# Kernel optimization log

Measured on AMD Instinct MI355X. Metric: run time of the kernel, lower is better.

The kernel has to match this reference:

```python
import jax, jax.numpy as jnp
import numpy as np

T, B, A, I, H, L = 256, 64, 512, 1024, 1024, 2
STDV = 1.0 / np.sqrt(H)

def _uniform(key, shape):
    return jax.random.uniform(key, shape, jnp.float32, -STDV, STDV)

def setup_inputs() -> dict:
    key = jax.random.key(0)
    ks = jax.random.split(key, 11)
    return {
        "attention": jax.random.normal(ks[0], (T, B, A), jnp.float32),
        "x": jax.random.normal(ks[1], (T, B, I), jnp.float32),
        "ping": jax.random.normal(ks[2], (B,), jnp.float32),  # unused by module
        "h0": jax.random.normal(ks[3], (L, B, H), jnp.float32),
        "c0": jax.random.normal(ks[4], (L, B, H), jnp.float32),
        "weight_ah": _uniform(ks[5], (L, A, 4 * H)),
        "weight_ih": _uniform(ks[6], (L, I, 4 * H)),  # input_size == hidden_size so layers stack
        "weight_hh": _uniform(ks[7], (L, H, 4 * H)),
        "bias_ah": _uniform(ks[8], (L, 4 * H)),
        "bias_ih": _uniform(ks[9], (L, 4 * H)),
        "bias_hh": _uniform(ks[10], (L, 4 * H)),
    }

def reference(attention, x, ping, h0, c0, weight_ah, weight_ih, weight_hh, bias_ah, bias_ih, bias_hh):
    # Faithful to SACILSTM.forward: only attention[0] is used (fixed across t),
    # ping is unused; per layer l, state is initialized from init_states[l].
    a0 = attention[0]  # [B, A]
    inputs = x  # [T, B, I]
    h_lasts, c_lasts = [], []
    for l in range(h0.shape[0]):
        w_hh = weight_hh[l]
        # Precompute the time-invariant + input-dependent part of the gates.
        const = a0 @ weight_ah[l] + bias_ah[l] + bias_ih[l] + bias_hh[l]  # [B, 4H]
        xg = jnp.einsum('tbi,ij->tbj', inputs, weight_ih[l]) + const  # [T, B, 4H]

        def step(carry, xg_t):
            h, c = carry
            gates = xg_t + h @ w_hh
            i_g, f_g, g_g, o_g = jnp.split(gates, 4, axis=-1)
            c = jax.nn.sigmoid(f_g) * c + jax.nn.sigmoid(i_g) * jnp.tanh(g_g)
            h = jax.nn.sigmoid(o_g) * jnp.tanh(c)
            return (h, c), h

        (h_T, c_T), hs = jax.lax.scan(step, (h0[l], c0[l]), xg)
        inputs = hs  # [T, B, H] feeds next layer
        h_lasts.append(h_T)
        c_lasts.append(c_T)
    # (self.h[:, -1], (self.h[-1], self.c[-1])) flattened
    return hs, jnp.stack(h_lasts), jnp.stack(c_lasts)
```

## Files before the change

### kernel.cpp

```cpp
#include <hip/hip_runtime.h>
#include <hip/hip_bf16.h>
#include <stdint.h>

#define TT 256
#define BB 64
#define AA 512
#define II 1024
#define HH 1024
#define LL 2
#define BH 65536
#define B4H 262144
#define OUT_HL 16777216
#define OUT_CL (16777216 + 131072)
#define NBLK 256

typedef __attribute__((ext_vector_type(8))) short bf16x8;
typedef __attribute__((ext_vector_type(4))) float f32x4;
typedef __attribute__((ext_vector_type(4))) unsigned int u32x4;
typedef __attribute__((ext_vector_type(2))) unsigned int u32x2;

__device__ __forceinline__ ushort f2bf(float v) {
    union { float f; uint32_t u; } x; x.f = v;
    uint32_t r = x.u + 0x7fff + ((x.u >> 16) & 1);
    return (ushort)(r >> 16);
}

__device__ __forceinline__ float sigf(float x) {
    return 1.f / (1.f + __expf(-x));
}


__global__ __launch_bounds__(256) void k_prep_wt(const float* __restrict__ wih,
                                                 const float* __restrict__ whh,
                                                 ushort* __restrict__ Wt) {
    __shared__ ushort tile[64][65];
    const int l = blockIdx.z;
    const int k0 = blockIdx.x * 64;
    const int col0 = blockIdx.y * 64;
    const int tid = threadIdx.x;
    const int cl = tid & 63, ks = tid >> 6;
    const float* src;
    int krow0;
    if (k0 < 1024) { src = wih + (size_t)l * 1024 * 4096; krow0 = k0; }
    else           { src = whh + (size_t)l * 1024 * 4096; krow0 = k0 - 1024; }
#pragma unroll
    for (int i = 0; i < 16; ++i) {
        int kl = ks + i * 4;
        tile[kl][cl] = f2bf(src[(size_t)(krow0 + kl) * 4096 + col0 + cl]);
    }
    __syncthreads();
    const int g0 = col0 >> 10, ub = col0 & 1023;
    ushort* dst = Wt + (size_t)l * 4096 * 2048;
    const int klane = tid & 63;
#pragma unroll
    for (int i = 0; i < 16; ++i) {
        int cl2 = (tid >> 6) + i * 4;
        int row = (ub + cl2) * 4 + g0;
        ushort* p = dst + (size_t)row * 2048 + k0 + klane;
        uint v = (uint)tile[klane][cl2];
        asm volatile("global_store_short %0, %1, off sc0 sc1"
                     :: "v"(p), "v"(v) : "memory");
    }
}

__global__ __launch_bounds__(256) void k_cast_x(const float* __restrict__ x,
                                                ushort* __restrict__ xbfF) {
    int i = blockIdx.x * 256 + threadIdx.x;
    int k8 = i & 127, b = (i >> 7) & 63, t = i >> 13;
    const float4* xs = (const float4*)(x + (((size_t)t * 64 + b) * 1024 + k8 * 8));
    float4 a = xs[0], c = xs[1];
    uint4 pk;
    pk.x = (uint)f2bf(a.x) | ((uint)f2bf(a.y) << 16);
    pk.y = (uint)f2bf(a.z) | ((uint)f2bf(a.w) << 16);
    pk.z = (uint)f2bf(c.x) | ((uint)f2bf(c.y) << 16);
    pk.w = (uint)f2bf(c.z) | ((uint)f2bf(c.w) << 16);
    size_t off = (size_t)t * 65536 + (size_t)(b >> 4) * 16384 +
                 (size_t)(k8 >> 2) * 512 + (size_t)(k8 & 3) * 128 + (size_t)(b & 15) * 8;
    *(uint4*)(xbfF + off) = pk;
}

__global__ __launch_bounds__(256) void k_const(const float* __restrict__ attn,
                                               const float* __restrict__ wah,
                                               const float* __restrict__ bah,
                                               const float* __restrict__ bih,
                                               const float* __restrict__ bhh,
                                               float* __restrict__ constg) {
    const int tid = threadIdx.x;
    const int col = blockIdx.x * 256 + tid;
    const int b0 = blockIdx.y * 8;
    const int l = blockIdx.z;
    const float* W = wah + (size_t)l * 512 * 4096;
    float acc[8] = {0.f, 0.f, 0.f, 0.f, 0.f, 0.f, 0.f, 0.f};
    for (int k = 0; k < 512; ++k) {
        float wv = W[(size_t)k * 4096 + col];
#pragma unroll
        for (int j = 0; j < 8; ++j) acc[j] += attn[(b0 + j) * 512 + k] * wv;
    }
    float bias = bah[l * 4096 + col] + bih[l * 4096 + col] + bhh[l * 4096 + col];
    float* cg = constg + (size_t)l * B4H;
#pragma unroll
    for (int j = 0; j < 8; ++j) cg[(size_t)(b0 + j) * 4096 + col] = acc[j] + bias;
}

__global__ __launch_bounds__(256) void k_init(const float* __restrict__ h0,
                                              ushort* __restrict__ hs0F,
                                              ushort* __restrict__ h1s0,
                                              unsigned* __restrict__ flags) {
    int i = blockIdx.x * 256 + threadIdx.x;
    if (i < 16384) {
        int k8 = i & 127, b = (i >> 7) & 63, l = i >> 13;
        const float* src = h0 + ((size_t)(l * 64 + b) * 1024 + k8 * 8);
        uint4 pk;
        pk.x = (uint)f2bf(src[0]) | ((uint)f2bf(src[1]) << 16);
        pk.y = (uint)f2bf(src[2]) | ((uint)f2bf(src[3]) << 16);
        pk.z = (uint)f2bf(src[4]) | ((uint)f2bf(src[5]) << 16);
        pk.w = (uint)f2bf(src[6]) | ((uint)f2bf(src[7]) << 16);
        size_t off = (size_t)(b >> 4) * 16384 + (size_t)(k8 >> 2) * 512 +
                     (size_t)(k8 & 3) * 128 + (size_t)(b & 15) * 8;
        *(uint4*)((l == 0 ? hs0F : h1s0) + off) = pk;
    }
    if (i < NBLK) flags[i] = 0u;
}

#define ISSUE(BUF, BASE)                                                       \
    do {                                                                       \
        _Pragma("unroll")                                                      \
        for (int _i = 0; _i < 8; ++_i)                                         \
            asm volatile("global_load_dwordx4 %0, %1, off"                     \
                         : "=v"(BUF[_i]) : "v"((BASE) + _i * 512));            \
    } while (0)

#define CHUNK(BUF, KTG0, N, A0, A1)                                            \
    do {                                                                       \
        asm volatile("s_waitcnt vmcnt(" #N ")" ::: "memory");                  \
        __builtin_amdgcn_sched_barrier(0x100);                                 \
        _Pragma("unroll")                                                      \
        for (int _i = 0; _i < 8; ++_i) {                                       \
            int _ktg = (KTG0) + _i;                                            \
            bf16x8 _b0 = *(const bf16x8*)(wlds + (size_t)_ktg * 1024 + lane * 8);       \
            bf16x8 _b1 = *(const bf16x8*)(wlds + (size_t)_ktg * 1024 + 512 + lane * 8); \
            A0 = __builtin_amdgcn_mfma_f32_16x16x32_bf16(BUF[_i], _b0, A0, 0, 0, 0);    \
            A1 = __builtin_amdgcn_mfma_f32_16x16x32_bf16(BUF[_i], _b1, A1, 0, 0, 0);    \
        }                                                                      \
    } while (0)

#define POLL128(FB, TGT)                                                       \
    do {                                                                       \
        const unsigned* _fp = (FB) + lane * 2;                                 \
        while (true) {                                                         \
            u32x2 _f;                                                          \
            asm volatile("global_load_dwordx2 %0, %1, off sc0 sc1\n\t"         \
                         "s_waitcnt vmcnt(0)"                                  \
                         : "=v"(_f) : "v"(_fp) : "memory");                    \
            if (__all(_f.x >= (TGT) && _f.y >= (TGT))) break;                  \
            __builtin_amdgcn_s_sleep(1);                                       \
        }                                                                      \
    } while (0)

__global__ __launch_bounds__(512, 2) void k_persist(
        const ushort* __restrict__ xbfF,
        ushort* __restrict__ hs0F,
        const ushort* __restrict__ h1s0,
        ushort* Wt,
        const float* __restrict__ constg,
        const float* __restrict__ c0,
        float* __restrict__ out,
        unsigned* __restrict__ flags) {
    __shared__ ushort wlds[65536];
    __shared__ float gt[2][4][2][16][18];

    const int tid = threadIdx.x;
    const int w = tid >> 6, lane = tid & 63;
    const int kh = w >> 2, m = w & 3;
    const int bid = blockIdx.x;
    const int layer = bid >> 7, ub = bid & 127;
    const int u0g = ub * 8;

    {
        bf16x8 vst[16];
#pragma unroll
        for (int i = 0; i < 16; ++i) {
            int c = i * 512 + tid;
            int lp = c & 63, nt = (c >> 6) & 1, ktg = c >> 7;
            int colp = u0g * 4 + nt * 16 + (lp & 15);
            int kk = ktg * 32 + (lp >> 4) * 8;
            const ushort* src = Wt + ((size_t)(layer * 4096 + colp)) * 2048 + kk;
            asm volatile("global_load_dwordx4 %0, %1, off sc0 sc1"
                         : "=v"(vst[i]) : "v"(src));
        }
        asm volatile("s_waitcnt vmcnt(0)" ::: "memory");
        __builtin_amdgcn_sched_barrier(0);
#pragma unroll
        for (int i = 0; i < 16; ++i) {
            int c = i * 512 + tid;
            *(bf16x8*)(wlds + (size_t)c * 8) = vst[i];
        }
    }

    const int b_e = (w << 3) | (lane >> 3);
    const int u_off = lane & 7;
    const int u_e = u0g + u_off;
    float cg[4];
#pragma unroll
    for (int g = 0; g < 4; ++g)
        cg[g] = constg[(size_t)layer * B4H + (size_t)b_e * 4096 + g * 1024 + u_e];
    float creg = c0[layer * BH + b_e * 1024 + u_e];
    const int mb = b_e >> 4, blb = b_e & 15, ntb = u_off >> 2, cpb = (u_off & 3) * 4;
    const size_t hoffL = (size_t)mb * 16384 + (size_t)(ub >> 2) * 512 +
                         (size_t)(ub & 3) * 128 + (size_t)blb * 8;

    const size_t fro = (size_t)m * 16384 + (size_t)lane * 8;

    __syncthreads();

    const int sBeg = layer ? 1 : 0;
    const int sEnd = layer ? TT : (TT - 1);
    for (int s = sBeg; s <= sEnd; ++s) {
        const int t1 = s - 1;
        bf16x8 bufA[8], bufB[8], bufC[8], bufD[8];
        f32x4 aE0 = {0.f,0.f,0.f,0.f}, aO0 = {0.f,0.f,0.f,0.f};
        f32x4 aE1 = {0.f,0.f,0.f,0.f}, aO1 = {0.f,0.f,0.f,0.f};

        if (layer == 0) {
            {
                const ushort* ax = xbfF + (size_t)s * 65536 + fro + kh * 8192;
                ISSUE(bufA, ax);
                ISSUE(bufB, ax + 4096);
                CHUNK(bufA, kh * 16,     8, aE0, aE1);
                CHUNK(bufB, kh * 16 + 8, 0, aO0, aO1);
            }
            if (s >= 1 && w == 0) POLL128(flags, (unsigned)s);
            __syncthreads();
            {
                const ushort* ah = hs0F + (size_t)s * 65536 + fro + kh * 8192;
                ISSUE(bufA, ah);
                ISSUE(bufB, ah + 4096);
                CHUNK(bufA, 32 + kh * 16,     8, aE0, aE1);
                CHUNK(bufB, 32 + kh * 16 + 8, 0, aO0, aO1);
            }
        } else {
            if (w == 0) POLL128(flags, (unsigned)s);
            if (w == 4 && s >= 2) POLL128(flags + 128, (unsigned)s);
            __syncthreads();
            {
                const ushort* a = (kh == 0)
                    ? hs0F + (size_t)s * 65536 + fro
                    : (t1 == 0 ? h1s0 + fro
                               : (const ushort*)Wt + (size_t)(t1 - 1) * 65536 + fro);
                ISSUE(bufA, a);
                ISSUE(bufB, a + 4096);
                ISSUE(bufC, a + 8192);
                ISSUE(bufD, a + 12288);
                CHUNK(bufA, kh * 32,      24, aE0, aE1);
                CHUNK(bufB, kh * 32 + 8,  16, aO0, aO1);
                CHUNK(bufC, kh * 32 + 16,  8, aE0, aE1);
                CHUNK(bufD, kh * 32 + 24,  0, aO0, aO1);
            }
        }

        {
            const int cc = lane & 15, r0 = (lane >> 4) * 4;
#pragma unroll
            for (int r = 0; r < 4; ++r) {
                gt[kh][m][0][r0 + r][cc] = aE0[r] + aO0[r];
                gt[kh][m][1][r0 + r][cc] = aE1[r] + aO1[r];
            }
        }
        __syncthreads();

        float g4[4];
#pragma unroll
        for (int g = 0; g < 4; ++g)
            g4[g] = gt[0][mb][ntb][blb][cpb + g] + gt[1][mb][ntb][blb][cpb + g] + cg[g];
        float si = sigf(g4[0]), sf = sigf(g4[1]), so = sigf(g4[3]);
        float cn = sf * creg + si * (2.f * sigf(2.f * g4[2]) - 1.f);
        float hv = so * (2.f * sigf(2.f * cn) - 1.f);
        creg = cn;
        uint hb = (uint)f2bf(hv);
        uint p0 = __shfl(hb, (lane & 56) + 0), p1 = __shfl(hb, (lane & 56) + 1);
        uint p2 = __shfl(hb, (lane & 56) + 2), p3 = __shfl(hb, (lane & 56) + 3);
        uint p4 = __shfl(hb, (lane & 56) + 4), p5 = __shfl(hb, (lane & 56) + 5);
        uint p6 = __shfl(hb, (lane & 56) + 6), p7 = __shfl(hb, (lane & 56) + 7);
        u32x4 hp;
        hp.x = (p0 & 0xffffu) | (p1 << 16);
        hp.y = (p2 & 0xffffu) | (p3 << 16);
        hp.z = (p4 & 0xffffu) | (p5 << 16);
        hp.w = (p6 & 0xffffu) | (p7 << 16);
        ushort* hdst = (layer ? Wt + (size_t)t1 * 65536
                              : hs0F + (size_t)(s + 1) * 65536) + hoffL;
        if (u_off == 0)
            asm volatile("global_store_dwordx4 %0, %1, off sc0 sc1"
                         :: "v"(hdst), "v"(hp) : "memory");

        asm volatile("s_waitcnt vmcnt(0)" ::: "memory");
        __syncthreads();
        if (tid == 0) {
            unsigned tgt = (unsigned)(s + 1);
            unsigned* fp = flags + layer * 128 + ub;
            asm volatile("global_store_dword %0, %1, off sc0 sc1"
                         :: "v"(fp), "v"(tgt) : "memory");
        }

        if (layer == 1) {
            float o0 = __shfl(hv, (lane & 56) + 0), o1 = __shfl(hv, (lane & 56) + 1);
            float o2 = __shfl(hv, (lane & 56) + 2), o3 = __shfl(hv, (lane & 56) + 3);
            float o4 = __shfl(hv, (lane & 56) + 4), o5 = __shfl(hv, (lane & 56) + 5);
            float o6 = __shfl(hv, (lane & 56) + 6), o7 = __shfl(hv, (lane & 56) + 7);
            if (u_off == 0) {
                float* op = out + (size_t)t1 * 65536 + (size_t)b_e * 1024 + u0g;
                float4 v0 = {o0, o1, o2, o3}, v1 = {o4, o5, o6, o7};
                *(float4*)op = v0;
                *(float4*)(op + 4) = v1;
            }
            if (t1 == TT - 1) {
                out[OUT_HL + BH + b_e * 1024 + u_e] = hv;
                out[OUT_CL + BH + b_e * 1024 + u_e] = cn;
            }
        } else if (s == TT - 1) {
            out[OUT_HL + b_e * 1024 + u_e] = hv;
            out[OUT_CL + b_e * 1024 + u_e] = cn;
        }
    }
}

extern "C" void kernel_launch(void* const* d_in, const int* in_sizes, int n_in,
                              void* d_out, int out_size, void* d_ws, size_t ws_size,
                              hipStream_t stream) {
    const float* attn = (const float*)d_in[0];
    const float* x    = (const float*)d_in[1];
    const float* h0   = (const float*)d_in[3];
    const float* c0   = (const float*)d_in[4];
    const float* wah  = (const float*)d_in[5];
    const float* wih  = (const float*)d_in[6];
    const float* whh  = (const float*)d_in[7];
    const float* bah  = (const float*)d_in[8];
    const float* bih  = (const float*)d_in[9];
    const float* bhh  = (const float*)d_in[10];
    float* out = (float*)d_out;

    char* ws = (char*)d_ws;
    ushort*   Wt     = (ushort*)(ws);
    ushort*   xbfF   = (ushort*)(ws + 33554432);
    ushort*   hs0F   = (ushort*)(ws + 67108864);
    ushort*   h1s0   = (ushort*)(ws + 100794368);
    float*    constg = (float*)(ws + 100925440);
    unsigned* flags  = (unsigned*)(ws + 103022592);

    hipLaunchKernelGGL(k_prep_wt, dim3(32, 64, 2), dim3(256), 0, stream, wih, whh, Wt);
    hipLaunchKernelGGL(k_cast_x, dim3(8192), dim3(256), 0, stream, x, xbfF);
    hipLaunchKernelGGL(k_const, dim3(16, 8, 2), dim3(256), 0, stream, attn, wah, bah, bih, bhh, constg);
    hipLaunchKernelGGL(k_init, dim3(64), dim3(256), 0, stream, h0, hs0F, h1s0, flags);

    void* args[] = { (void*)&xbfF, (void*)&hs0F, (void*)&h1s0, (void*)&Wt,
                     (void*)&constg, (void*)&c0, (void*)&out, (void*)&flags };
    hipLaunchCooperativeKernel((void*)k_persist, dim3(NBLK), dim3(512), args, 0, stream);
}
```

Baseline: 1.681 ms.

## Split persistent LSTM into four roles, decoupling input-projection blocks from recurrent blocks

The persistent kernel now gives 256 blocks four roles: input-projection producers for each layer (x@Wih and h0@Wih) that write fp32 gate partials into ring buffers, and recurrent blocks that only compute h@Whh and the cell update. Weights are loaded into shared memory once at kernel start. The ring buffers reuse the Wt workspace region, and new flag arrays handle ring-slot backpressure and a startup barrier so blocks only overwrite Wt after every block has loaded its weights. The intent is to take the input GEMM off the serial recurrent critical path so each recurrent step does half the K-work. The cost is more flag polling, extra global traffic for the fp32 partials, and fragile ordering around the aliased workspace.

Measured after the change: 2.199 ms. 1.31x slower.

```diff
diff --git a/kernel.cpp b/kernel.cpp
--- a/kernel.cpp
+++ b/kernel.cpp
@@ -3,31 +3,24 @@
 #include <stdint.h>
 
 #define TT 256
-#define BB 64
-#define AA 512
-#define II 1024
-#define HH 1024
-#define LL 2
 #define BH 65536
 #define B4H 262144
 #define OUT_HL 16777216
 #define OUT_CL (16777216 + 131072)
 #define NBLK 256
+#define SLAB 65536
+#define XGSZ 262144
 
 typedef __attribute__((ext_vector_type(8))) short bf16x8;
 typedef __attribute__((ext_vector_type(4))) float f32x4;
 typedef __attribute__((ext_vector_type(4))) unsigned int u32x4;
-typedef __attribute__((ext_vector_type(2))) unsigned int u32x2;
 
 __device__ __forceinline__ ushort f2bf(float v) {
     union { float f; uint32_t u; } x; x.f = v;
     uint32_t r = x.u + 0x7fff + ((x.u >> 16) & 1);
     return (ushort)(r >> 16);
 }
-
-__device__ __forceinline__ float sigf(float x) {
-    return 1.f / (1.f + __expf(-x));
-}
+__device__ __forceinline__ float sigf(float x) { return 1.f / (1.f + __expf(-x)); }
 
 
 __global__ __launch_bounds__(256) void k_prep_wt(const float* __restrict__ wih,
@@ -74,7 +67,7 @@
     pk.y = (uint)f2bf(a.z) | ((uint)f2bf(a.w) << 16);
     pk.z = (uint)f2bf(c.x) | ((uint)f2bf(c.y) << 16);
     pk.w = (uint)f2bf(c.z) | ((uint)f2bf(c.w) << 16);
-    size_t off = (size_t)t * 65536 + (size_t)(b >> 4) * 16384 +
+    size_t off = (size_t)t * SLAB + (size_t)(b >> 4) * 16384 +
                  (size_t)(k8 >> 2) * 512 + (size_t)(k8 & 3) * 128 + (size_t)(b & 15) * 8;
     *(uint4*)(xbfF + off) = pk;
 }
@@ -119,72 +112,98 @@
                      (size_t)(k8 & 3) * 128 + (size_t)(b & 15) * 8;
         *(uint4*)((l == 0 ? hs0F : h1s0) + off) = pk;
     }
-    if (i < NBLK) flags[i] = 0u;
-}
-
-#define ISSUE(BUF, BASE)                                                       \
-    do {                                                                       \
-        _Pragma("unroll")                                                      \
+    if (i < 512) flags[i] = 0u;
+}
+
+#define ISSUE8(BUF, BASE)                                                      \
+    do { _Pragma("unroll")                                                     \
         for (int _i = 0; _i < 8; ++_i)                                         \
             asm volatile("global_load_dwordx4 %0, %1, off"                     \
-                         : "=v"(BUF[_i]) : "v"((BASE) + _i * 512));            \
-    } while (0)
-
-#define CHUNK(BUF, KTG0, N, A0, A1)                                            \
+                         : "=v"(BUF[_i]) : "v"((BASE) + _i * 512)); } while (0)
+#define ISSUE8_SC(BUF, BASE)                                                   \
+    do { _Pragma("unroll")                                                     \
+        for (int _i = 0; _i < 8; ++_i)                                         \
+            asm volatile("global_load_dwordx4 %0, %1, off sc0 sc1"             \
+                         : "=v"(BUF[_i]) : "v"((BASE) + _i * 512)); } while (0)
+
+#define MFMA(A, B, C) __builtin_amdgcn_mfma_f32_16x16x32_bf16(A, B, C, 0, 0, 0)
+
+#define CHUNK8(BUF, KTG0, N)                                                   \
     do {                                                                       \
         asm volatile("s_waitcnt vmcnt(" #N ")" ::: "memory");                  \
         __builtin_amdgcn_sched_barrier(0x100);                                 \
         _Pragma("unroll")                                                      \
         for (int _i = 0; _i < 8; ++_i) {                                       \
-            int _ktg = (KTG0) + _i;                                            \
-            bf16x8 _b0 = *(const bf16x8*)(wlds + (size_t)_ktg * 1024 + lane * 8);       \
-            bf16x8 _b1 = *(const bf16x8*)(wlds + (size_t)_ktg * 1024 + 512 + lane * 8); \
-            A0 = __builtin_amdgcn_mfma_f32_16x16x32_bf16(BUF[_i], _b0, A0, 0, 0, 0);    \
-            A1 = __builtin_amdgcn_mfma_f32_16x16x32_bf16(BUF[_i], _b1, A1, 0, 0, 0);    \
+            const ushort* _wb = wlds + ((size_t)((KTG0) + _i) * 256 + lane) * 8; \
+            bf16x8 _b0 = *(const bf16x8*)(_wb);                                \
+            bf16x8 _b1 = *(const bf16x8*)(_wb + 512);                          \
+            bf16x8 _b2 = *(const bf16x8*)(_wb + 1024);                         \
+            bf16x8 _b3 = *(const bf16x8*)(_wb + 1536);                         \
+            acc0 = MFMA(BUF[_i], _b0, acc0);                                   \
+            acc1 = MFMA(BUF[_i], _b1, acc1);                                   \
+            acc2 = MFMA(BUF[_i], _b2, acc2);                                   \
+            acc3 = MFMA(BUF[_i], _b3, acc3);                                   \
         }                                                                      \
     } while (0)
 
-#define POLL128(FB, TGT)                                                       \
-    do {                                                                       \
-        const unsigned* _fp = (FB) + lane * 2;                                 \
-        while (true) {                                                         \
-            u32x2 _f;                                                          \
-            asm volatile("global_load_dwordx2 %0, %1, off sc0 sc1\n\t"         \
-                         "s_waitcnt vmcnt(0)"                                  \
-                         : "=v"(_f) : "v"(_fp) : "memory");                    \
-            if (__all(_f.x >= (TGT) && _f.y >= (TGT))) break;                  \
-            __builtin_amdgcn_s_sleep(1);                                       \
-        }                                                                      \
-    } while (0)
+#define POLLALL64(FB, TGT)                                                     \
+    do { const unsigned* _fp = (FB) + lane;                                    \
+        while (true) { unsigned _f;                                            \
+            asm volatile("global_load_dword %0, %1, off sc0 sc1\n\t"           \
+                         "s_waitcnt vmcnt(0)" : "=v"(_f) : "v"(_fp) : "memory"); \
+            if (__all(_f >= (unsigned)(TGT))) break;                           \
+            __builtin_amdgcn_s_sleep(1); } } while (0)
+
+#define POLLONE(FP, TGT)                                                       \
+    do { while (true) { unsigned _f;                                           \
+            asm volatile("global_load_dword %0, %1, off sc0 sc1\n\t"           \
+                         "s_waitcnt vmcnt(0)" : "=v"(_f) : "v"(FP) : "memory"); \
+            if (_f >= (unsigned)(TGT)) break;                                  \
+            __builtin_amdgcn_s_sleep(1); } } while (0)
+
+#define POLLS256(FB)                                                           \
+    do { const unsigned* _fp = (FB) + lane * 4;                                \
+        while (true) { u32x4 _f;                                               \
+            asm volatile("global_load_dwordx4 %0, %1, off sc0 sc1\n\t"         \
+                         "s_waitcnt vmcnt(0)" : "=v"(_f) : "v"(_fp) : "memory"); \
+            if (__all(_f.x && _f.y && _f.z && _f.w)) break;                    \
+            __builtin_amdgcn_s_sleep(1); } } while (0)
 
 __global__ __launch_bounds__(512, 2) void k_persist(
-        const ushort* __restrict__ xbfF,
-        ushort* __restrict__ hs0F,
+        ushort* xbfF,
+        ushort* hs0F,
         const ushort* __restrict__ h1s0,
-        ushort* Wt,
+        const ushort* __restrict__ Wt,
         const float* __restrict__ constg,
         const float* __restrict__ c0,
         float* __restrict__ out,
-        unsigned* __restrict__ flags) {
+        unsigned* flags,
+        float* xg0, float* xg1) {
     __shared__ ushort wlds[65536];
-    __shared__ float gt[2][4][2][16][18];
+    __shared__ float gt[4][16][68];
 
     const int tid = threadIdx.x;
     const int w = tid >> 6, lane = tid & 63;
     const int kh = w >> 2, m = w & 3;
     const int bid = blockIdx.x;
-    const int layer = bid >> 7, ub = bid & 127;
-    const int u0g = ub * 8;
+    const int role = bid >> 6, j = bid & 63;
+    const int lsel = role >> 1;
+    const int hbase = (role & 1) * 1024;
+    unsigned* fS  = flags;
+    unsigned* fAp = flags + 256;
+    unsigned* fA  = flags + 320;
+    unsigned* fB  = flags + 384;
+    unsigned* fC  = flags + 448;
 
     {
         bf16x8 vst[16];
 #pragma unroll
         for (int i = 0; i < 16; ++i) {
             int c = i * 512 + tid;
-            int lp = c & 63, nt = (c >> 6) & 1, ktg = c >> 7;
-            int colp = u0g * 4 + nt * 16 + (lp & 15);
-            int kk = ktg * 32 + (lp >> 4) * 8;
-            const ushort* src = Wt + ((size_t)(layer * 4096 + colp)) * 2048 + kk;
+            int ktg = c >> 8, nt = (c >> 6) & 3, lp = c & 63;
+            int colp = 64 * j + nt * 16 + (lp & 15);
+            int kk = hbase + ktg * 32 + (lp >> 4) * 8;
+            const ushort* src = Wt + ((size_t)(lsel * 4096 + colp)) * 2048 + kk;
             asm volatile("global_load_dwordx4 %0, %1, off sc0 sc1"
                          : "=v"(vst[i]) : "v"(src));
         }
@@ -196,129 +215,174 @@
             *(bf16x8*)(wlds + (size_t)c * 8) = vst[i];
         }
     }
-
-    const int b_e = (w << 3) | (lane >> 3);
-    const int u_off = lane & 7;
-    const int u_e = u0g + u_off;
-    float cg[4];
-#pragma unroll
-    for (int g = 0; g < 4; ++g)
-        cg[g] = constg[(size_t)layer * B4H + (size_t)b_e * 4096 + g * 1024 + u_e];
-    float creg = c0[layer * BH + b_e * 1024 + u_e];
-    const int mb = b_e >> 4, blb = b_e & 15, ntb = u_off >> 2, cpb = (u_off & 3) * 4;
-    const size_t hoffL = (size_t)mb * 16384 + (size_t)(ub >> 2) * 512 +
-                         (size_t)(ub & 3) * 128 + (size_t)blb * 8;
-
-    const size_t fro = (size_t)m * 16384 + (size_t)lane * 8;
-
     __syncthreads();
-
-    const int sBeg = layer ? 1 : 0;
-    const int sEnd = layer ? TT : (TT - 1);
-    for (int s = sBeg; s <= sEnd; ++s) {
-        const int t1 = s - 1;
-        bf16x8 bufA[8], bufB[8], bufC[8], bufD[8];
-        f32x4 aE0 = {0.f,0.f,0.f,0.f}, aO0 = {0.f,0.f,0.f,0.f};
-        f32x4 aE1 = {0.f,0.f,0.f,0.f}, aO1 = {0.f,0.f,0.f,0.f};
-
-        if (layer == 0) {
-            {
-                const ushort* ax = xbfF + (size_t)s * 65536 + fro + kh * 8192;
-                ISSUE(bufA, ax);
-                ISSUE(bufB, ax + 4096);
-                CHUNK(bufA, kh * 16,     8, aE0, aE1);
-                CHUNK(bufB, kh * 16 + 8, 0, aO0, aO1);
-            }
-            if (s >= 1 && w == 0) POLL128(flags, (unsigned)s);
-            __syncthreads();
-            {
-                const ushort* ah = hs0F + (size_t)s * 65536 + fro + kh * 8192;
-                ISSUE(bufA, ah);
-                ISSUE(bufB, ah + 4096);
-                CHUNK(bufA, 32 + kh * 16,     8, aE0, aE1);
-                CHUNK(bufB, 32 + kh * 16 + 8, 0, aO0, aO1);
+    if (tid == 0) {
+        unsigned one = 1u; unsigned* fp = fS + bid;
+        asm volatile("global_store_dword %0, %1, off sc0 sc1"
+                     :: "v"(fp), "v"(one) : "memory");
+    }
+
+    const int cc = lane & 15, r0 = (lane >> 4) * 4;
+    f32x4 cst0 = {0,0,0,0}, cst1 = {0,0,0,0}, cst2 = {0,0,0,0}, cst3 = {0,0,0,0};
+    if (role == 0 || role == 2) {
+#pragma unroll
+        for (int nt = 0; nt < 4; ++nt) {
+            int colp = nt * 16 + cc;
+            size_t base = (size_t)lsel * B4H + (size_t)(cc & 3) * 1024 + 16 * j + (colp >> 2);
+            f32x4 v;
+#pragma unroll
+            for (int r = 0; r < 4; ++r)
+                v[r] = constg[base + (size_t)(m * 16 + r0 + r) * 4096];
+            if (nt == 0) cst0 = v; else if (nt == 1) cst1 = v;
+            else if (nt == 2) cst2 = v; else cst3 = v;
+        }
+    }
+    const int b_e = tid >> 3, p_e = tid & 7, up = p_e * 2;
+    const int ug0 = 16 * j + up;
+    float cregA = 0.f, cregB = 0.f;
+    size_t hoffT = 0;
+    if (role == 1 || role == 3) {
+        cregA = c0[lsel * BH + b_e * 1024 + ug0];
+        cregB = c0[lsel * BH + b_e * 1024 + ug0 + 1];
+        hoffT = (size_t)(b_e >> 4) * 16384 + (size_t)(ug0 >> 5) * 512 +
+                (size_t)((ug0 >> 3) & 3) * 128 + (size_t)(b_e & 15) * 8 + (ug0 & 7);
+    }
+    const size_t fro = (size_t)m * 16384 + (size_t)(kh * 16) * 512 + (size_t)lane * 8;
+    __syncthreads();
+
+    for (int t = 0; t < TT; ++t) {
+        f32x4 acc0 = {0,0,0,0}, acc1 = {0,0,0,0}, acc2 = {0,0,0,0}, acc3 = {0,0,0,0};
+        bf16x8 bufA[8], bufB[8];
+        float xgv[8];
+
+        if (role == 1) {
+            if (w == 0) POLLALL64(fA, t);
+            if (w == 1) POLLONE(fAp + j, t + 1);
+            __syncthreads();
+        } else if (role == 2) {
+            if (w == 0) POLLALL64(fA, t + 1);
+            if (w == 1 && t >= 7) POLLONE(fC + j, t - 6);
+            __syncthreads();
+        } else if (role == 3) {
+            if (w == 0) POLLALL64(fC, t);
+            if (w == 1) POLLONE(fB + j, t + 1);
+            __syncthreads();
+        }
+
+        if (role == 1 || role == 3) {
+            const float* xg = (role == 1) ? xg0 + (size_t)(t & 15) * XGSZ
+                                          : xg1 + (size_t)(t & 7) * XGSZ;
+#pragma unroll
+            for (int e = 0; e < 2; ++e)
+#pragma unroll
+                for (int g = 0; g < 4; ++g) {
+                    const float* p = xg + (size_t)((64 * j + (up + e) * 4 + g)) * 64 + b_e;
+                    asm volatile("global_load_dword %0, %1, off sc0 sc1"
+                                 : "=v"(xgv[e * 4 + g]) : "v"(p));
+                }
+        }
+
+        {
+            const ushort* slab;
+            if (role == 0)      slab = xbfF + (size_t)t * SLAB;
+            else if (role == 1) slab = hs0F + (size_t)t * SLAB;
+            else if (role == 2) slab = hs0F + (size_t)(t + 1) * SLAB;
+            else                slab = (t == 0) ? h1s0 : xbfF + (size_t)(t - 1) * SLAB;
+            const ushort* base = slab + fro;
+            if (role == 0) { ISSUE8_SC(bufA, base); ISSUE8_SC(bufB, base + 4096); }
+            else           { ISSUE8(bufA, base);    ISSUE8(bufB, base + 4096); }
+            CHUNK8(bufA, kh * 16, 8);
+            CHUNK8(bufB, kh * 16 + 8, 0);
+        }
+
+        if (kh == 1) {
+#pragma unroll
+            for (int r = 0; r < 4; ++r) {
+                gt[m][r0 + r][0 * 16 + cc] = acc0[r];
+                gt[m][r0 + r][1 * 16 + cc] = acc1[r];
+                gt[m][r0 + r][2 * 16 + cc] = acc2[r];
+                gt[m][r0 + r][3 * 16 + cc] = acc3[r];
+            }
+        }
+        if (role == 0) {
+            if (w == 0 && t == 0) POLLS256(fS);
+            if (w == 0 && t >= 15) POLLONE(fA + j, t - 14);
+        }
+        __syncthreads();
+
+        if (role == 0 || role == 2) {
+            if (kh == 0) {
+                float* dst = (role == 0 ? xg0 + (size_t)(t & 15) * XGSZ
+                                        : xg1 + (size_t)(t & 7) * XGSZ);
+#pragma unroll
+                for (int nt = 0; nt < 4; ++nt) {
+                    f32x4 a = (nt == 0) ? acc0 : (nt == 1) ? acc1 : (nt == 2) ? acc2 : acc3;
+                    f32x4 cs = (nt == 0) ? cst0 : (nt == 1) ? cst1 : (nt == 2) ? cst2 : cst3;
+                    f32x4 v;
+#pragma unroll
+                    for (int r = 0; r < 4; ++r)
+                        v[r] = a[r] + gt[m][r0 + r][nt * 16 + cc] + cs[r];
+                    float* ap = dst + (size_t)(64 * j + nt * 16 + cc) * 64 + m * 16 + r0;
+                    asm volatile("global_store_dwordx4 %0, %1, off sc0 sc1"
+                                 :: "v"(ap), "v"(v) : "memory");
+                }
+            }
+            asm volatile("s_waitcnt vmcnt(0)" ::: "memory");
+            __syncthreads();
+            if (tid == 0) {
+                unsigned tgt = (unsigned)(t + 1);
+                unsigned* fp = (role == 0 ? fAp : fB) + j;
+                asm volatile("global_store_dword %0, %1, off sc0 sc1"
+                             :: "v"(fp), "v"(tgt) : "memory");
             }
         } else {
-            if (w == 0) POLL128(flags, (unsigned)s);
-            if (w == 4 && s >= 2) POLL128(flags + 128, (unsigned)s);
-            __syncthreads();
-            {
-                const ushort* a = (kh == 0)
-                    ? hs0F + (size_t)s * 65536 + fro
-                    : (t1 == 0 ? h1s0 + fro
-                               : (const ushort*)Wt + (size_t)(t1 - 1) * 65536 + fro);
-                ISSUE(bufA, a);
-                ISSUE(bufB, a + 4096);
-                ISSUE(bufC, a + 8192);
-                ISSUE(bufD, a + 12288);
-                CHUNK(bufA, kh * 32,      24, aE0, aE1);
-                CHUNK(bufB, kh * 32 + 8,  16, aO0, aO1);
-                CHUNK(bufC, kh * 32 + 16,  8, aE0, aE1);
-                CHUNK(bufD, kh * 32 + 24,  0, aO0, aO1);
-            }
-        }
-
-        {
-            const int cc = lane & 15, r0 = (lane >> 4) * 4;
-#pragma unroll
-            for (int r = 0; r < 4; ++r) {
-                gt[kh][m][0][r0 + r][cc] = aE0[r] + aO0[r];
-                gt[kh][m][1][r0 + r][cc] = aE1[r] + aO1[r];
-            }
-        }
-        __syncthreads();
-
-        float g4[4];
-#pragma unroll
-        for (int g = 0; g < 4; ++g)
-            g4[g] = gt[0][mb][ntb][blb][cpb + g] + gt[1][mb][ntb][blb][cpb + g] + cg[g];
-        float si = sigf(g4[0]), sf = sigf(g4[1]), so = sigf(g4[3]);
-        float cn = sf * creg + si * (2.f * sigf(2.f * g4[2]) - 1.f);
-        float hv = so * (2.f * sigf(2.f * cn) - 1.f);
-        creg = cn;
-        uint hb = (uint)f2bf(hv);
-        uint p0 = __shfl(hb, (lane & 56) + 0), p1 = __shfl(hb, (lane & 56) + 1);
-        uint p2 = __shfl(hb, (lane & 56) + 2), p3 = __shfl(hb, (lane & 56) + 3);
-        uint p4 = __shfl(hb, (lane & 56) + 4), p5 = __shfl(hb, (lane & 56) + 5);
-        uint p6 = __shfl(hb, (lane & 56) + 6), p7 = __shfl(hb, (lane & 56) + 7);
-        u32x4 hp;
-        hp.x = (p0 & 0xffffu) | (p1 << 16);
-        hp.y = (p2 & 0xffffu) | (p3 << 16);
-        hp.z = (p4 & 0xffffu) | (p5 << 16);
-        hp.w = (p6 & 0xffffu) | (p7 << 16);
-        ushort* hdst = (layer ? Wt + (size_t)t1 * 65536
-                              : hs0F + (size_t)(s + 1) * 65536) + hoffL;
-        if (u_off == 0)
-            asm volatile("global_store_dwordx4 %0, %1, off sc0 sc1"
-                         :: "v"(hdst), "v"(hp) : "memory");
-
-        asm volatile("s_waitcnt vmcnt(0)" ::: "memory");
-        __syncthreads();
-        if (tid == 0) {
-            unsigned tgt = (unsigned)(s + 1);
-            unsigned* fp = flags + layer * 128 + ub;
+            if (kh == 0) {
+#pragma unroll
+                for (int r = 0; r < 4; ++r) {
+                    gt[m][r0 + r][0 * 16 + cc] += acc0[r];
+                    gt[m][r0 + r][1 * 16 + cc] += acc1[r];
+                    gt[m][r0 + r][2 * 16 + cc] += acc2[r];
+                    gt[m][r0 + r][3 * 16 + cc] += acc3[r];
+                }
+            }
+            __syncthreads();
+            f32x4 va = *(const f32x4*)&gt[b_e >> 4][b_e & 15][up * 4];
+            f32x4 vb = *(const f32x4*)&gt[b_e >> 4][b_e & 15][up * 4 + 4];
+            float giA = va[0] + xgv[0], gfA = va[1] + xgv[1];
+            float ggA = va[2] + xgv[2], goA = va[3] + xgv[3];
+            float giB = vb[0] + xgv[4], gfB = vb[1] + xgv[5];
+            float ggB = vb[2] + xgv[6], goB = vb[3] + xgv[7];
+            float cnA = sigf(gfA) * cregA + sigf(giA) * (2.f * sigf(2.f * ggA) - 1.f);
+            float hvA = sigf(goA) * (2.f * sigf(2.f * cnA) - 1.f);
+            float cnB = sigf(gfB) * cregB + sigf(giB) * (2.f * sigf(2.f * ggB) - 1.f);
+            float hvB = sigf(goB) * (2.f * sigf(2.f * cnB) - 1.f);
+            cregA = cnA; cregB = cnB;
+            uint hb = (uint)f2bf(hvA) | ((uint)f2bf(hvB) << 16);
+            ushort* hdst = (role == 1 ? hs0F + (size_t)(t + 1) * SLAB
+                                      : xbfF + (size_t)t * SLAB) + hoffT;
             asm volatile("global_store_dword %0, %1, off sc0 sc1"
-                         :: "v"(fp), "v"(tgt) : "memory");
-        }
-
-        if (layer == 1) {
-            float o0 = __shfl(hv, (lane & 56) + 0), o1 = __shfl(hv, (lane & 56) + 1);
-            float o2 = __shfl(hv, (lane & 56) + 2), o3 = __shfl(hv, (lane & 56) + 3);
-            float o4 = __shfl(hv, (lane & 56) + 4), o5 = __shfl(hv, (lane & 56) + 5);
-            float o6 = __shfl(hv, (lane & 56) + 6), o7 = __shfl(hv, (lane & 56) + 7);
-            if (u_off == 0) {
-                float* op = out + (size_t)t1 * 65536 + (size_t)b_e * 1024 + u0g;
-                float4 v0 = {o0, o1, o2, o3}, v1 = {o4, o5, o6, o7};
-                *(float4*)op = v0;
-                *(float4*)(op + 4) = v1;
-            }
-            if (t1 == TT - 1) {
-                out[OUT_HL + BH + b_e * 1024 + u_e] = hv;
-                out[OUT_CL + BH + b_e * 1024 + u_e] = cn;
-            }
-        } else if (s == TT - 1) {
-            out[OUT_HL + b_e * 1024 + u_e] = hv;
-            out[OUT_CL + b_e * 1024 + u_e] = cn;
+                         :: "v"(hdst), "v"(hb) : "memory");
+            asm volatile("s_waitcnt vmcnt(0)" ::: "memory");
+            __syncthreads();
+            if (tid == 0) {
+                unsigned tgt = (unsigned)(t + 1);
+                unsigned* fp = (role == 1 ? fA : fC) + j;
+                asm volatile("global_store_dword %0, %1, off sc0 sc1"
+                             :: "v"(fp), "v"(tgt) : "memory");
+            }
+            if (role == 3) {
+                float2 ov; ov.x = hvA; ov.y = hvB;
+                *(float2*)(out + (size_t)t * BH + (size_t)b_e * 1024 + ug0) = ov;
+                if (t == TT - 1) {
+                    int idx = b_e * 1024 + ug0;
+                    out[OUT_HL + BH + idx] = hvA; out[OUT_HL + BH + idx + 1] = hvB;
+                    out[OUT_CL + BH + idx] = cnA; out[OUT_CL + BH + idx + 1] = cnB;
+                }
+            } else if (t == TT - 1) {
+                int idx = b_e * 1024 + ug0;
+                out[OUT_HL + idx] = hvA; out[OUT_HL + idx + 1] = hvB;
+                out[OUT_CL + idx] = cnA; out[OUT_CL + idx + 1] = cnB;
+            }
         }
     }
 }
@@ -340,6 +404,8 @@
 
     char* ws = (char*)d_ws;
     ushort*   Wt     = (ushort*)(ws);
+    float*    xg0    = (float*)(ws);
+    float*    xg1    = (float*)(ws + 16777216);
     ushort*   xbfF   = (ushort*)(ws + 33554432);
     ushort*   hs0F   = (ushort*)(ws + 67108864);
     ushort*   h1s0   = (ushort*)(ws + 100794368);
@@ -352,6 +418,7 @@
     hipLaunchKernelGGL(k_init, dim3(64), dim3(256), 0, stream, h0, hs0F, h1s0, flags);
 
     void* args[] = { (void*)&xbfF, (void*)&hs0F, (void*)&h1s0, (void*)&Wt,
-                     (void*)&constg, (void*)&c0, (void*)&out, (void*)&flags };
+                     (void*)&constg, (void*)&c0, (void*)&out, (void*)&flags,
+                     (void*)&xg0, (void*)&xg1 };
     hipLaunchCooperativeKernel((void*)k_persist, dim3(NBLK), dim3(512), args, 0, stream);
 }
```

## Split LSTM recurrence per layer and prefetch next-step operands across barriers

Applied to the files above, without the earlier changes.

The persistent recurrent kernel is split into separate loops for layer 0 and layer 1. Each loop issues the loads for the next step's operands early: the next x slab in layer 0, and the freshly published layer-0 h in layer 1. This lets those loads overlap with the current step's MFMA work and flag polling, and the k-split is reorganized so each half reads input and recurrent operands in separate register buffers. It adds register pressure from four live buffer sets. The layer-1 waits are also restructured, with two separate polls per step, which could change synchronization latency.

After: 2.064 ms. +22.8%, slower.

```diff
diff --git a/kernel.cpp b/kernel.cpp
--- a/kernel.cpp
+++ b/kernel.cpp
@@ -3,16 +3,12 @@
 #include <stdint.h>
 
 #define TT 256
-#define BB 64
-#define AA 512
-#define II 1024
-#define HH 1024
-#define LL 2
 #define BH 65536
 #define B4H 262144
 #define OUT_HL 16777216
 #define OUT_CL (16777216 + 131072)
 #define NBLK 256
+#define SLAB 65536
 
 typedef __attribute__((ext_vector_type(8))) short bf16x8;
 typedef __attribute__((ext_vector_type(4))) float f32x4;
@@ -24,10 +20,7 @@
     uint32_t r = x.u + 0x7fff + ((x.u >> 16) & 1);
     return (ushort)(r >> 16);
 }
-
-__device__ __forceinline__ float sigf(float x) {
-    return 1.f / (1.f + __expf(-x));
-}
+__device__ __forceinline__ float sigf(float x) { return 1.f / (1.f + __expf(-x)); }
 
 
 __global__ __launch_bounds__(256) void k_prep_wt(const float* __restrict__ wih,
@@ -74,7 +67,7 @@
     pk.y = (uint)f2bf(a.z) | ((uint)f2bf(a.w) << 16);
     pk.z = (uint)f2bf(c.x) | ((uint)f2bf(c.y) << 16);
     pk.w = (uint)f2bf(c.z) | ((uint)f2bf(c.w) << 16);
-    size_t off = (size_t)t * 65536 + (size_t)(b >> 4) * 16384 +
+    size_t off = (size_t)t * SLAB + (size_t)(b >> 4) * 16384 +
                  (size_t)(k8 >> 2) * 512 + (size_t)(k8 & 3) * 128 + (size_t)(b & 15) * 8;
     *(uint4*)(xbfF + off) = pk;
 }
@@ -123,12 +116,10 @@
 }
 
 #define ISSUE(BUF, BASE)                                                       \
-    do {                                                                       \
-        _Pragma("unroll")                                                      \
+    do { _Pragma("unroll")                                                     \
         for (int _i = 0; _i < 8; ++_i)                                         \
             asm volatile("global_load_dwordx4 %0, %1, off"                     \
-                         : "=v"(BUF[_i]) : "v"((BASE) + _i * 512));            \
-    } while (0)
+                         : "=v"(BUF[_i]) : "v"((BASE) + _i * 512)); } while (0)
 
 #define CHUNK(BUF, KTG0, N, A0, A1)                                            \
     do {                                                                       \
@@ -209,116 +200,160 @@
     const size_t hoffL = (size_t)mb * 16384 + (size_t)(ub >> 2) * 512 +
                          (size_t)(ub & 3) * 128 + (size_t)blb * 8;
 
-    const size_t fro = (size_t)m * 16384 + (size_t)lane * 8;
+    const size_t fro = (size_t)m * 16384 + (size_t)(kh * 16) * 512 + (size_t)lane * 8;
+    unsigned* f0 = flags;
+    unsigned* f1 = flags + 128;
 
     __syncthreads();
 
-    const int sBeg = layer ? 1 : 0;
-    const int sEnd = layer ? TT : (TT - 1);
-    for (int s = sBeg; s <= sEnd; ++s) {
-        const int t1 = s - 1;
-        bf16x8 bufA[8], bufB[8], bufC[8], bufD[8];
-        f32x4 aE0 = {0.f,0.f,0.f,0.f}, aO0 = {0.f,0.f,0.f,0.f};
-        f32x4 aE1 = {0.f,0.f,0.f,0.f}, aO1 = {0.f,0.f,0.f,0.f};
-
-        if (layer == 0) {
+    bf16x8 bufXa[8], bufXb[8];
+    bf16x8 bufHa[8], bufHb[8];
+
+    if (layer == 0) {
+        { const ushort* ax = xbfF + fro; ISSUE(bufXa, ax); ISSUE(bufXb, ax + 4096); }
+        { const ushort* ah = hs0F + fro; ISSUE(bufHa, ah); ISSUE(bufHb, ah + 4096); }
+        for (int s = 0; s < TT; ++s) {
+            f32x4 aE0 = {0,0,0,0}, aO0 = {0,0,0,0};
+            f32x4 aE1 = {0,0,0,0}, aO1 = {0,0,0,0};
+            CHUNK(bufXa, kh * 16,     16, aE0, aE1);
+            CHUNK(bufXb, kh * 16 + 8, 16, aO0, aO1);
+            { const ushort* ax = xbfF + (size_t)((s + 1) & 255) * SLAB + fro;
+              ISSUE(bufXa, ax); ISSUE(bufXb, ax + 4096); }
+            CHUNK(bufHa, 32 + kh * 16,     24, aE0, aE1);
+            CHUNK(bufHb, 32 + kh * 16 + 8, 16, aO0, aO1);
             {
-                const ushort* ax = xbfF + (size_t)s * 65536 + fro + kh * 8192;
-                ISSUE(bufA, ax);
-                ISSUE(bufB, ax + 4096);
-                CHUNK(bufA, kh * 16,     8, aE0, aE1);
-                CHUNK(bufB, kh * 16 + 8, 0, aO0, aO1);
-            }
-            if (s >= 1 && w == 0) POLL128(flags, (unsigned)s);
+                const int cc = lane & 15, r0 = (lane >> 4) * 4;
+#pragma unroll
+                for (int r = 0; r < 4; ++r) {
+                    gt[kh][m][0][r0 + r][cc] = aE0[r] + aO0[r];
+                    gt[kh][m][1][r0 + r][cc] = aE1[r] + aO1[r];
+                }
+            }
             __syncthreads();
+            float g4[4];
+#pragma unroll
+            for (int g = 0; g < 4; ++g)
+                g4[g] = gt[0][mb][ntb][blb][cpb + g] + gt[1][mb][ntb][blb][cpb + g] + cg[g];
+            float si = sigf(g4[0]), sf = sigf(g4[1]), so = sigf(g4[3]);
+            float cn = sf * creg + si * (2.f * sigf(2.f * g4[2]) - 1.f);
+            float hv = so * (2.f * sigf(2.f * cn) - 1.f);
+            creg = cn;
+            uint hb = (uint)f2bf(hv);
+            uint p0 = __shfl(hb, (lane & 56) + 0), p1 = __shfl(hb, (lane & 56) + 1);
+            uint p2 = __shfl(hb, (lane & 56) + 2), p3 = __shfl(hb, (lane & 56) + 3);
+            uint p4 = __shfl(hb, (lane & 56) + 4), p5 = __shfl(hb, (lane & 56) + 5);
+            uint p6 = __shfl(hb, (lane & 56) + 6), p7 = __shfl(hb, (lane & 56) + 7);
+            u32x4 hp;
+            hp.x = (p0 & 0xffffu) | (p1 << 16);
+            hp.y = (p2 & 0xffffu) | (p3 << 16);
+            hp.z = (p4 & 0xffffu) | (p5 << 16);
+            hp.w = (p6 & 0xffffu) | (p7 << 16);
+            ushort* hdst = hs0F + (size_t)(s + 1) * SLAB + hoffL;
+            if (u_off == 0)
+                asm volatile("global_store_dwordx4 %0, %1, off sc0 sc1"
+                             :: "v"(hdst), "v"(hp) : "memory");
+            asm volatile("s_waitcnt vmcnt(0)" ::: "memory");
+            __syncthreads();
+            if (tid == 0) {
+                unsigned tgt = (unsigned)(s + 1);
+                unsigned* fp = f0 + ub;
+                asm volatile("global_store_dword %0, %1, off sc0 sc1"
+                             :: "v"(fp), "v"(tgt) : "memory");
+            }
+            if (s == TT - 1) {
+                int idx = b_e * 1024 + u_e;
+                out[OUT_HL + idx] = hv;
+                out[OUT_CL + idx] = cn;
+            }
+            if (s < TT - 1) {
+                if (w == 0) POLL128(f0, (unsigned)(s + 1));
+                __syncthreads();
+                const ushort* ah = hs0F + (size_t)(s + 1) * SLAB + fro;
+                ISSUE(bufHa, ah); ISSUE(bufHb, ah + 4096);
+            }
+        }
+    } else {
+        if (w == 0) POLL128(f0, 1u);
+        __syncthreads();
+        { const ushort* ah = hs0F + (size_t)1 * SLAB + fro;
+          ISSUE(bufHa, ah); ISSUE(bufHb, ah + 4096); }
+        for (int s = 1; s <= TT; ++s) {
+            const int t1 = s - 1;
+            f32x4 aE0 = {0,0,0,0}, aO0 = {0,0,0,0};
+            f32x4 aE1 = {0,0,0,0}, aO1 = {0,0,0,0};
+            if (s >= 2) {
+                if (w == 0) POLL128(f1, (unsigned)s);
+                __syncthreads();
+            }
+            { const ushort* ar = (t1 == 0 ? h1s0
+                                 : (const ushort*)Wt + (size_t)(t1 - 1) * SLAB) + fro;
+              ISSUE(bufXa, ar); ISSUE(bufXb, ar + 4096); }
+            CHUNK(bufHa, kh * 16,          24, aE0, aE1);
+            CHUNK(bufHb, kh * 16 + 8,      16, aO0, aO1);
+            CHUNK(bufXa, 32 + kh * 16,      8, aE0, aE1);
+            CHUNK(bufXb, 32 + kh * 16 + 8,  0, aO0, aO1);
             {
-                const ushort* ah = hs0F + (size_t)s * 65536 + fro + kh * 8192;
-                ISSUE(bufA, ah);
-                ISSUE(bufB, ah + 4096);
-                CHUNK(bufA, 32 + kh * 16,     8, aE0, aE1);
-                CHUNK(bufB, 32 + kh * 16 + 8, 0, aO0, aO1);
-            }
-        } else {
-            if (w == 0) POLL128(flags, (unsigned)s);
-            if (w == 4 && s >= 2) POLL128(flags + 128, (unsigned)s);
+                const int cc = lane & 15, r0 = (lane >> 4) * 4;
+#pragma unroll
+                for (int r = 0; r < 4; ++r) {
+                    gt[kh][m][0][r0 + r][cc] = aE0[r] + aO0[r];
+                    gt[kh][m][1][r0 + r][cc] = aE1[r] + aO1[r];
+                }
+            }
             __syncthreads();
+            float g4[4];
+#pragma unroll
+            for (int g = 0; g < 4; ++g)
+                g4[g] = gt[0][mb][ntb][blb][cpb + g] + gt[1][mb][ntb][blb][cpb + g] + cg[g];
+            float si = sigf(g4[0]), sf = sigf(g4[1]), so = sigf(g4[3]);
+            float cn = sf * creg + si * (2.f * sigf(2.f * g4[2]) - 1.f);
+            float hv = so * (2.f * sigf(2.f * cn) - 1.f);
+            creg = cn;
+            uint hb = (uint)f2bf(hv);
+            uint p0 = __shfl(hb, (lane & 56) + 0), p1 = __shfl(hb, (lane & 56) + 1);
+            uint p2 = __shfl(hb, (lane & 56) + 2), p3 = __shfl(hb, (lane & 56) + 3);
+            uint p4 = __shfl(hb, (lane & 56) + 4), p5 = __shfl(hb, (lane & 56) + 5);
+            uint p6 = __shfl(hb, (lane & 56) + 6), p7 = __shfl(hb, (lane & 56) + 7);
+            u32x4 hp;
+            hp.x = (p0 & 0xffffu) | (p1 << 16);
+            hp.y = (p2 & 0xffffu) | (p3 << 16);
+            hp.z = (p4 & 0xffffu) | (p5 << 16);
+            hp.w = (p6 & 0xffffu) | (p7 << 16);
+            ushort* hdst = Wt + (size_t)t1 * SLAB + hoffL;
+            if (u_off == 0)
+                asm volatile("global_store_dwordx4 %0, %1, off sc0 sc1"
+                             :: "v"(hdst), "v"(hp) : "memory");
+            asm volatile("s_waitcnt vmcnt(0)" ::: "memory");
+            __syncthreads();
+            if (tid == 0) {
+                unsigned tgt = (unsigned)(s + 1);
+                unsigned* fp = f1 + ub;
+                asm volatile("global_store_dword %0, %1, off sc0 sc1"
+                             :: "v"(fp), "v"(tgt) : "memory");
+            }
             {
-                const ushort* a = (kh == 0)
-                    ? hs0F + (size_t)s * 65536 + fro
-                    : (t1 == 0 ? h1s0 + fro
-                               : (const ushort*)Wt + (size_t)(t1 - 1) * 65536 + fro);
-                ISSUE(bufA, a);
-                ISSUE(bufB, a + 4096);
-                ISSUE(bufC, a + 8192);
-                ISSUE(bufD, a + 12288);
-                CHUNK(bufA, kh * 32,      24, aE0, aE1);
-                CHUNK(bufB, kh * 32 + 8,  16, aO0, aO1);
-                CHUNK(bufC, kh * 32 + 16,  8, aE0, aE1);
-                CHUNK(bufD, kh * 32 + 24,  0, aO0, aO1);
-            }
-        }
-
-        {
-            const int cc = lane & 15, r0 = (lane >> 4) * 4;
-#pragma unroll
-            for (int r = 0; r < 4; ++r) {
-                gt[kh][m][0][r0 + r][cc] = aE0[r] + aO0[r];
-                gt[kh][m][1][r0 + r][cc] = aE1[r] + aO1[r];
-            }
-        }
-        __syncthreads();
-
-        float g4[4];
-#pragma unroll
-        for (int g = 0; g < 4; ++g)
-            g4[g] = gt[0][mb][ntb][blb][cpb + g] + gt[1][mb][ntb][blb][cpb + g] + cg[g];
-        float si = sigf(g4[0]), sf = sigf(g4[1]), so = sigf(g4[3]);
-        float cn = sf * creg + si * (2.f * sigf(2.f * g4[2]) - 1.f);
-        float hv = so * (2.f * sigf(2.f * cn) - 1.f);
-        creg = cn;
-        uint hb = (uint)f2bf(hv);
-        uint p0 = __shfl(hb, (lane & 56) + 0), p1 = __shfl(hb, (lane & 56) + 1);
-        uint p2 = __shfl(hb, (lane & 56) + 2), p3 = __shfl(hb, (lane & 56) + 3);
-        uint p4 = __shfl(hb, (lane & 56) + 4), p5 = __shfl(hb, (lane & 56) + 5);
-        uint p6 = __shfl(hb, (lane & 56) + 6), p7 = __shfl(hb, (lane & 56) + 7);
-        u32x4 hp;
-        hp.x = (p0 & 0xffffu) | (p1 << 16);
-        hp.y = (p2 & 0xffffu) | (p3 << 16);
-        hp.z = (p4 & 0xffffu) | (p5 << 16);
-        hp.w = (p6 & 0xffffu) | (p7 << 16);
-        ushort* hdst = (layer ? Wt + (size_t)t1 * 65536
-                              : hs0F + (size_t)(s + 1) * 65536) + hoffL;
-        if (u_off == 0)
-            asm volatile("global_store_dwordx4 %0, %1, off sc0 sc1"
-                         :: "v"(hdst), "v"(hp) : "memory");
-
-        asm volatile("s_waitcnt vmcnt(0)" ::: "memory");
-        __syncthreads();
-        if (tid == 0) {
-            unsigned tgt = (unsigned)(s + 1);
-            unsigned* fp = flags + layer * 128 + ub;
-            asm volatile("global_store_dword %0, %1, off sc0 sc1"
-                         :: "v"(fp), "v"(tgt) : "memory");
-        }
-
-        if (layer == 1) {
-            float o0 = __shfl(hv, (lane & 56) + 0), o1 = __shfl(hv, (lane & 56) + 1);
-            float o2 = __shfl(hv, (lane & 56) + 2), o3 = __shfl(hv, (lane & 56) + 3);
-            float o4 = __shfl(hv, (lane & 56) + 4), o5 = __shfl(hv, (lane & 56) + 5);
-            float o6 = __shfl(hv, (lane & 56) + 6), o7 = __shfl(hv, (lane & 56) + 7);
-            if (u_off == 0) {
-                float* op = out + (size_t)t1 * 65536 + (size_t)b_e * 1024 + u0g;
-                float4 v0 = {o0, o1, o2, o3}, v1 = {o4, o5, o6, o7};
-                *(float4*)op = v0;
-                *(float4*)(op + 4) = v1;
-            }
-            if (t1 == TT - 1) {
-                out[OUT_HL + BH + b_e * 1024 + u_e] = hv;
-                out[OUT_CL + BH + b_e * 1024 + u_e] = cn;
-            }
-        } else if (s == TT - 1) {
-            out[OUT_HL + b_e * 1024 + u_e] = hv;
-            out[OUT_CL + b_e * 1024 + u_e] = cn;
+                float o0 = __shfl(hv, (lane & 56) + 0), o1 = __shfl(hv, (lane & 56) + 1);
+                float o2 = __shfl(hv, (lane & 56) + 2), o3 = __shfl(hv, (lane & 56) + 3);
+                float o4 = __shfl(hv, (lane & 56) + 4), o5 = __shfl(hv, (lane & 56) + 5);
+                float o6 = __shfl(hv, (lane & 56) + 6), o7 = __shfl(hv, (lane & 56) + 7);
+                if (u_off == 0) {
+                    float* op = out + (size_t)t1 * BH + (size_t)b_e * 1024 + u0g;
+                    float4 v0 = {o0, o1, o2, o3}, v1 = {o4, o5, o6, o7};
+                    *(float4*)op = v0;
+                    *(float4*)(op + 4) = v1;
+                }
+                if (t1 == TT - 1) {
+                    int idx = b_e * 1024 + u_e;
+                    out[OUT_HL + BH + idx] = hv;
+                    out[OUT_CL + BH + idx] = cn;
+                }
+            }
+            if (s < TT) {
+                if (w == 0) POLL128(f0, (unsigned)(s + 1));
+                __syncthreads();
+                const ushort* ah = hs0F + (size_t)(s + 1) * SLAB + fro;
+                ISSUE(bufHa, ah); ISSUE(bufHb, ah + 4096);
+            }
         }
     }
 }
```
